# Optimization experiments

Hardware: AMD Instinct MI355X
Metric: run time of the kernel (lower is better)

The kernel has to match this reference:

```python
import jax, jax.numpy as jnp
import numpy as np

N_USER, N_ITEM, D, K, E = 80000, 40000, 128, 10, 2000000

def _mlp(x, w1, b1, w2, b2, w3, b3):
    # MLP from source: linear->tanh->linear->tanh->linear->L2 normalize (eval mode, dropout off)
    x = jnp.tanh(x @ w1 + b1)
    x = jnp.tanh(x @ w2 + b2)
    x = x @ w3 + b3
    return x / jnp.maximum(jnp.linalg.norm(x, axis=-1, keepdims=True), 1e-12)

def setup_inputs() -> dict:
    key = jax.random.key(0)
    ks = jax.random.split(key, 24)
    s = 0.05
    inp = {
        'uemb_s': jax.random.normal(ks[0], (N_USER, D), jnp.float32),
        'iemb_s': jax.random.normal(ks[1], (N_ITEM, D), jnp.float32),
        'uemb_t': jax.random.normal(ks[2], (N_USER, D), jnp.float32),
        'u_emb_sp': jax.random.normal(ks[3], (N_USER, D), jnp.float32),
        'edge_user': jax.random.randint(ks[4], (E,), 0, N_USER, jnp.int32),
        'edge_item': jax.random.randint(ks[5], (E,), 0, N_ITEM, jnp.int32),
        # meta nets
        'Wu': jax.random.normal(ks[6], (4 * D, D), jnp.float32) * s,
        'bu': jnp.zeros((D,), jnp.float32),
        'Wi': jax.random.normal(ks[7], (2 * D, D), jnp.float32) * s,
        'bi': jnp.zeros((D,), jnp.float32),
        # mlp1: D -> D*K -> D//2 -> D*K
        'm1w1': jax.random.normal(ks[8], (D, D * K), jnp.float32) * s,
        'm1b1': jnp.zeros((D * K,), jnp.float32),
        'm1w2': jax.random.normal(ks[9], (D * K, D // 2), jnp.float32) * s,
        'm1b2': jnp.zeros((D // 2,), jnp.float32),
        'm1w3': jax.random.normal(ks[10], (D // 2, D * K), jnp.float32) * s,
        'm1b3': jnp.zeros((D * K,), jnp.float32),
        # mlp2: D -> D*K -> D//2 -> D*K
        'm2w1': jax.random.normal(ks[11], (D, D * K), jnp.float32) * s,
        'm2b1': jnp.zeros((D * K,), jnp.float32),
        'm2w2': jax.random.normal(ks[12], (D * K, D // 2), jnp.float32) * s,
        'm2b2': jnp.zeros((D // 2,), jnp.float32),
        'm2w3': jax.random.normal(ks[13], (D // 2, D * K), jnp.float32) * s,
        'm2b3': jnp.zeros((D * K,), jnp.float32),
    }
    return inp

def reference(uemb_s, iemb_s, uemb_t, u_emb_sp, edge_user, edge_item,
              Wu, bu, Wi, bi,
              m1w1, m1b1, m1w2, m1b2, m1w3, m1b3,
              m2w1, m2b1, m2w2, m2b2, m2w3, m2b3):
    # spmm with all-ones values == gather + segment_sum over the bipartite edge list
    neighbors_u = jax.ops.segment_sum(iemb_s[edge_item], edge_user, num_segments=N_USER)  # [U, D]
    tmp_embu = jax.lax.stop_gradient(
        jnp.concatenate([uemb_s, uemb_t, u_emb_sp, neighbors_u], axis=1)) @ Wu + bu       # [U, D]
    neighbors_i = jax.ops.segment_sum(((uemb_s + u_emb_sp) * 0.5)[edge_user], edge_item,
                                      num_segments=N_ITEM)                               # [I, D]
    tmp_embi = jax.lax.stop_gradient(
        jnp.concatenate([iemb_s, neighbors_i], axis=1)) @ Wi + bi                         # [I, D]
    metau = _mlp(tmp_embu, m1w1, m1b1, m1w2, m1b2, m1w3, m1b3).reshape(-1, D, K)          # [U, D, K]
    metai = _mlp(tmp_embi, m2w1, m2b1, m2w2, m2b2, m2w3, m2b3).reshape(-1, K, D)          # [I, K, D]
    meta_biasu = jnp.mean(metau, axis=0)  # [D, K]
    meta_biasi = jnp.mean(metai, axis=0)  # [K, D]
    low_weightu = jax.nn.softmax(metau + meta_biasu, axis=1)
    low_weighti = jax.nn.softmax(metai + meta_biasi, axis=1)
    return (low_weightu, low_weighti)
```

## Files before the change

kernel.cpp:

```cpp
#include <hip/hip_runtime.h>
#include <hip/hip_bf16.h>

#define D_ 128
#define DK_ 1280
#define K_ 10

typedef __attribute__((ext_vector_type(8))) short bh8;
typedef __attribute__((ext_vector_type(4))) short bh4;
typedef __attribute__((ext_vector_type(4))) float f32x4;

__device__ __forceinline__ short f2b(float f) {
    unsigned u = __builtin_bit_cast(unsigned, f);
    u += 0x7fffu + ((u >> 16) & 1u);
    return (short)(u >> 16);
}
__device__ __forceinline__ float b2f(short s) {
    unsigned u = ((unsigned)(unsigned short)s) << 16;
    return __builtin_bit_cast(float, u);
}
__device__ __forceinline__ float tanh_fast(float x) {
    float e = __expf(2.f * x);
    return 1.f - __fdividef(2.f, e + 1.f);
}
__device__ __forceinline__ f32x4 mfma16(bh8 a, bh8 b, f32x4 c) {
    return __builtin_amdgcn_mfma_f32_16x16x32_bf16(a, b, c, 0, 0, 0);
}

__device__ __forceinline__ int blk_excl_scan(int v, int t) {
    __shared__ int wp[4];
    int lane = t & 63, w = t >> 6;
    int s = v;
    for (int o = 1; o < 64; o <<= 1) {
        int pv = __shfl_up(s, o);
        if (lane >= o) s += pv;
    }
    if (lane == 63) wp[w] = s;
    __syncthreads();
    if (t == 0) {
        int a = 0;
#pragma unroll
        for (int k = 0; k < 4; ++k) { int x = wp[k]; wp[k] = a; a += x; }
    }
    __syncthreads();
    int r = s - v + wp[w];
    __syncthreads();
    return r;
}

__global__ __launch_bounds__(256) void cvt_all(
    const float* __restrict__ us, const float* __restrict__ ut,
    const float* __restrict__ usp, const float* __restrict__ is_,
    short* __restrict__ usb, short* __restrict__ utb,
    short* __restrict__ uspb, short* __restrict__ uavg, short* __restrict__ isb,
    int n4u, int n4i)
{
    int i = blockIdx.x * 256 + threadIdx.x;
    if (i < n4u) {
        float4 a = ((const float4*)us)[i];
        float4 b = ((const float4*)ut)[i];
        float4 c = ((const float4*)usp)[i];
        bh4 sa, sb, sc, sv;
        sa[0] = f2b(a.x); sa[1] = f2b(a.y); sa[2] = f2b(a.z); sa[3] = f2b(a.w);
        sb[0] = f2b(b.x); sb[1] = f2b(b.y); sb[2] = f2b(b.z); sb[3] = f2b(b.w);
        sc[0] = f2b(c.x); sc[1] = f2b(c.y); sc[2] = f2b(c.z); sc[3] = f2b(c.w);
        sv[0] = f2b(0.5f * (a.x + c.x)); sv[1] = f2b(0.5f * (a.y + c.y));
        sv[2] = f2b(0.5f * (a.z + c.z)); sv[3] = f2b(0.5f * (a.w + c.w));
        ((bh4*)usb)[i] = sa; ((bh4*)utb)[i] = sb;
        ((bh4*)uspb)[i] = sc; ((bh4*)uavg)[i] = sv;
    } else if (i < n4u + n4i) {
        int j = i - n4u;
        float4 v = ((const float4*)is_)[j];
        bh4 s;
        s[0] = f2b(v.x); s[1] = f2b(v.y); s[2] = f2b(v.z); s[3] = f2b(v.w);
        ((bh4*)isb)[j] = s;
    }
}

struct PackArgs {
    const float* W[8];
    short* o[8];
    int K[8];
    int N[8];
};
__global__ __launch_bounds__(256) void pack_all(PackArgs pa)
{
    int seg = blockIdx.y;
    int K = pa.K[seg], N = pa.N[seg];
    int total = K * N;
    int o = blockIdx.x * 256 + threadIdx.x;
    if (o >= total) return;
    const float* W = pa.W[seg];
    short* out = pa.o[seg];
    int j    = o & 7;
    int lane = (o >> 3) & 63;
    int rest = o >> 9;
    int KK = K >> 5;
    int kk = rest % KK;
    int tile = rest / KK;
    int k = kk * 32 + (lane >> 4) * 8 + j;
    int n = tile * 16 + (lane & 15);
    out[o] = f2b(W[(size_t)k * N + n]);
}

__global__ __launch_bounds__(256) void bhist_kernel(
    const int* __restrict__ eu, const int* __restrict__ ei,
    int* __restrict__ bcu, int* __restrict__ bci,
    int E, int shu, int shi, int nbu, int nbi)
{
    __shared__ int hu[160], hi[160];
    int t = threadIdx.x;
    int base = blockIdx.x * 4096;
    if (t < 160) { hu[t] = 0; hi[t] = 0; }
    __syncthreads();
    int n = min(4096, E - base);
#pragma unroll 4
    for (int k = 0; k < 16; ++k) {
        int idx = k * 256 + t;
        if (idx < n) {
            atomicAdd(&hu[eu[base + idx] >> shu], 1);
            atomicAdd(&hi[ei[base + idx] >> shi], 1);
        }
    }
    __syncthreads();
    if (t < nbu && hu[t]) atomicAdd(&bcu[t], hu[t]);
    if (t < nbi && hi[t]) atomicAdd(&bci[t], hi[t]);
}

__global__ __launch_bounds__(256) void binit_kernel(
    const int* __restrict__ bcu, int* __restrict__ gcu, int* __restrict__ bbu, int nbu,
    const int* __restrict__ bci, int* __restrict__ gci, int* __restrict__ bbi, int nbi,
    int E)
{
    int t = threadIdx.x;
    {
        int v = (t < nbu) ? bcu[t] : 0;
        int ex = blk_excl_scan(v, t);
        if (t < nbu) { gcu[t] = ex; bbu[t] = ex; }
        if (t == 0) bbu[nbu] = E;
    }
    __syncthreads();
    {
        int v = (t < nbi) ? bci[t] : 0;
        int ex = blk_excl_scan(v, t);
        if (t < nbi) { gci[t] = ex; bbi[t] = ex; }
        if (t == 0) bbi[nbi] = E;
    }
}

__global__ __launch_bounds__(256) void partition_kernel(
    const int* __restrict__ eu, const int* __restrict__ ei,
    int* __restrict__ gcu, int* __restrict__ gci,
    uint2* __restrict__ ebu, uint2* __restrict__ ebi,
    int E, int shu, int shi, int nbu, int nbi)
{
    __shared__ int hu[160], hi[160];
    int t = threadIdx.x;
    int base = blockIdx.x * 4096;
    if (t < 160) { hu[t] = 0; hi[t] = 0; }
    __syncthreads();
    int n = min(4096, E - base);
    int us[16], is_[16];
#pragma unroll 4
    for (int k = 0; k < 16; ++k) {
        int idx = k * 256 + t;
        if (idx < n) {
            us[k] = eu[base + idx];
            is_[k] = ei[base + idx];
            atomicAdd(&hu[us[k] >> shu], 1);
            atomicAdd(&hi[is_[k] >> shi], 1);
        } else us[k] = -1;
    }
    __syncthreads();
    if (t < nbu) { int c = hu[t]; hu[t] = c ? atomicAdd(&gcu[t], c) : 0; }
    if (t < nbi) { int c = hi[t]; hi[t] = c ? atomicAdd(&gci[t], c) : 0; }
    __syncthreads();
#pragma unroll 4
    for (int k = 0; k < 16; ++k) {
        if (us[k] >= 0) {
            int p1 = atomicAdd(&hu[us[k] >> shu], 1);
            ebu[p1] = make_uint2((unsigned)us[k], (unsigned)is_[k]);
            int p2 = atomicAdd(&hi[is_[k] >> shi], 1);
            ebi[p2] = make_uint2((unsigned)is_[k], (unsigned)us[k]);
        }
    }
}

__global__ __launch_bounds__(256) void fill2_all(
    const uint2* __restrict__ ebu, const int* __restrict__ bbu,
    int* __restrict__ off_u, int* __restrict__ end_u, int* __restrict__ adj_u,
    int NBU, int U,
    const uint2* __restrict__ ebi, const int* __restrict__ bbi,
    int* __restrict__ off_i, int* __restrict__ end_i, int* __restrict__ adj_i, int I)
{
    __shared__ int lcnt[512];
    __shared__ int lcur[512];
    bool isU = (int)blockIdx.x < NBU;
    const uint2* ebuf = isU ? ebu : ebi;
    const int* bbase  = isU ? bbu : bbi;
    int* off  = isU ? off_u : off_i;
    int* end_ = isU ? end_u : end_i;
    int* adj  = isU ? adj_u : adj_i;
    int span_sh = isU ? 9 : 8;
    int nrows = isU ? U : I;
    int b = isU ? blockIdx.x : blockIdx.x - NBU;

    int t = threadIdx.x;
    int rbase = b << span_sh;
    int span = min(1 << span_sh, nrows - rbase);
    int regbeg = bbase[b], regend = bbase[b + 1];
    for (int j = t; j < span; j += 256) lcnt[j] = 0;
    __syncthreads();
    for (int e = regbeg + t; e < regend; e += 256)
        atomicAdd(&lcnt[ebuf[e].x - rbase], 1);
    __syncthreads();
    int c0 = (2 * t < span) ? lcnt[2 * t] : 0;
    int c1 = (2 * t + 1 < span) ? lcnt[2 * t + 1] : 0;
    int ex = blk_excl_scan(c0 + c1, t);
    if (2 * t < span) {
        int beg = regbeg + ex;
        off[rbase + 2 * t] = beg;
        end_[rbase + 2 * t] = beg + c0;
        lcur[2 * t] = beg;
    }
    if (2 * t + 1 < span) {
        int beg = regbeg + ex + c0;
        off[rbase + 2 * t + 1] = beg;
        end_[rbase + 2 * t + 1] = beg + c1;
        lcur[2 * t + 1] = beg;
    }
    __syncthreads();
    for (int e = regbeg + t; e < regend; e += 256) {
        uint2 p = ebuf[e];
        int slot = atomicAdd(&lcur[p.x - rbase], 1);
        adj[slot] = (int)p.y;
    }
}

__global__ __launch_bounds__(256) void gather_all(
    const short* __restrict__ embU, const short* __restrict__ embI,
    const int* __restrict__ off_u, const int* __restrict__ end_u, const int* __restrict__ adj_u,
    const int* __restrict__ off_i, const int* __restrict__ end_i, const int* __restrict__ adj_i,
    short* __restrict__ nub, short* __restrict__ nib, int U, int I)
{
    int gw = (blockIdx.x * 256 + threadIdx.x) >> 6;
    int lane = threadIdx.x & 63;
    const short* emb; const int *offp, *endp, *adjp; short* outp; int row;
    if (gw < U)          { emb = embU; offp = off_u; endp = end_u; adjp = adj_u; outp = nub; row = gw; }
    else if (gw < U + I) { emb = embI; offp = off_i; endp = end_i; adjp = adj_i; outp = nib; row = gw - U; }
    else return;

    int beg = offp[row], end = endp[row];
    float ax = 0.f, ay = 0.f;
    int j = beg;
    for (; j + 3 < end; j += 4) {
        unsigned a = *(const unsigned*)(emb + (size_t)adjp[j]     * D_ + lane * 2);
        unsigned b = *(const unsigned*)(emb + (size_t)adjp[j + 1] * D_ + lane * 2);
        unsigned c = *(const unsigned*)(emb + (size_t)adjp[j + 2] * D_ + lane * 2);
        unsigned d = *(const unsigned*)(emb + (size_t)adjp[j + 3] * D_ + lane * 2);
        ax += b2f((short)(a & 0xffff)) + b2f((short)(b & 0xffff))
            + b2f((short)(c & 0xffff)) + b2f((short)(d & 0xffff));
        ay += b2f((short)(a >> 16)) + b2f((short)(b >> 16))
            + b2f((short)(c >> 16)) + b2f((short)(d >> 16));
    }
    for (; j < end; ++j) {
        unsigned a = *(const unsigned*)(emb + (size_t)adjp[j] * D_ + lane * 2);
        ax += b2f((short)(a & 0xffff));
        ay += b2f((short)(a >> 16));
    }
    unsigned o = ((unsigned)(unsigned short)f2b(ay) << 16) | (unsigned short)(unsigned)f2b(ax);
    *(unsigned*)(outp + (size_t)row * D_ + lane * 2) = o;
}

struct MlpArgs {
    const short *uA0, *uA1, *uA2, *uA3;
    const short *iA0, *iA1;
    const short *uWg, *uW1, *uW2, *uW3;
    const short *iWg, *iW1, *iW2, *iW3;
    const float *ubg, *ub1, *ub2, *ub3;
    const float *ibg, *ib1, *ib2, *ib3;
    short *uY, *iY;
    int UB;
};

__global__ __launch_bounds__(256, 4) void fused_mlp_all(MlpArgs P)
{
    __shared__ char pool[27712];
    short* x2   = (short*)pool;
    short* h2   = (short*)(pool + 4352);
    float* wred = (float*)(pool + 6656);
    float* nrms = (float*)(pool + 6912);
    short* xc   = (short*)(pool + 6976);
    short* h1h  = (short*)(pool + 6976);

    const int t = threadIdx.x;
    const int l = t & 63;
    const int w = t >> 6;
    const int lr = l & 15;
    const int lg = l >> 4;

    const bool isU = (int)blockIdx.x < P.UB;
    const int bid = isU ? (int)blockIdx.x : (int)blockIdx.x - P.UB;
    const size_t rb0 = (size_t)bid * 16;
    const int CHSH = isU ? 6 : 5;
    const int KKG  = isU ? 16 : 8;
    const int XST  = isU ? 520 : 264;
    const short* Wg = isU ? P.uWg : P.iWg;
    const short* W1 = isU ? P.uW1 : P.iW1;
    const short* W2 = isU ? P.uW2 : P.iW2;
    const short* W3 = isU ? P.uW3 : P.iW3;
    const float* bg = isU ? P.ubg : P.ibg;
    const float* b1 = isU ? P.ub1 : P.ib1;
    const float* b2 = isU ? P.ub2 : P.ib2;
    const float* b3 = isU ? P.ub3 : P.ib3;
    short* Ybf = isU ? P.uY : P.iY;

    for (int idx = t; idx < (16 << CHSH); idx += 256) {
        int row = idx >> CHSH;
        int slot = idx & ((1 << CHSH) - 1);
        int a = slot >> 4, cs = slot & 15;
        const short* src = isU ? (a == 0 ? P.uA0 : a == 1 ? P.uA1 : a == 2 ? P.uA2 : P.uA3)
                               : (a == 0 ? P.iA0 : P.iA1);
        bh8 v = *(const bh8*)(src + (rb0 + row) * D_ + cs * 8);
        *(bh8*)(xc + row * XST + slot * 8) = v;
    }
    __syncthreads();

    {
        f32x4 a0 = {0,0,0,0}, b0 = a0, a1 = a0, b1v = a0;
        const short* wp = Wg + (size_t)(2 * w) * KKG * 512 + l * 8;
        const short* wq = wp + (size_t)KKG * 512;
        const short* xp = xc + lr * XST + lg * 8;
        for (int kk = 0; kk < KKG; ++kk) {
            bh8 xf = *(const bh8*)xp; xp += 32;
            bh8 w0 = *(const bh8*)wp; wp += 512;
            bh8 w1 = *(const bh8*)wq; wq += 512;
            if (kk & 1) { b0 = mfma16(w0, xf, b0); b1v = mfma16(w1, xf, b1v); }
            else        { a0 = mfma16(w0, xf, a0); a1 = mfma16(w1, xf, a1); }
        }
        float4 c0 = *(const float4*)(bg + (2 * w) * 16 + lg * 4);
        float4 c1 = *(const float4*)(bg + (2 * w + 1) * 16 + lg * 4);
        bh4 p0, p1;
        p0[0] = f2b(a0[0] + b0[0] + c0.x); p0[1] = f2b(a0[1] + b0[1] + c0.y);
        p0[2] = f2b(a0[2] + b0[2] + c0.z); p0[3] = f2b(a0[3] + b0[3] + c0.w);
        p1[0] = f2b(a1[0] + b1v[0] + c1.x); p1[1] = f2b(a1[1] + b1v[1] + c1.y);
        p1[2] = f2b(a1[2] + b1v[2] + c1.z); p1[3] = f2b(a1[3] + b1v[3] + c1.w);
        *(bh4*)(x2 + lr * 136 + (2 * w) * 16 + lg * 4) = p0;
        *(bh4*)(x2 + lr * 136 + (2 * w + 1) * 16 + lg * 4) = p1;
    }
    __syncthreads();

    bh8 xf[4];
#pragma unroll
    for (int kk = 0; kk < 4; ++kk)
        xf[kk] = *(const bh8*)(x2 + lr * 136 + kk * 32 + lg * 8);

    f32x4 c2a = {0,0,0,0}, c2b = c2a;
#pragma unroll 1
    for (int h = 0; h < 2; ++h) {
        const short* wp = W1 + (size_t)(h * 40 + w * 10) * 2048 + l * 8;
        const float* bp = b1 + (h * 40 + w * 10) * 16 + lg * 4;
        short* hp = h1h + lr * 648 + w * 160 + lg * 4;
#pragma unroll 2
        for (int tt = 0; tt < 10; ++tt) {
            f32x4 acc = {0, 0, 0, 0};
#pragma unroll
            for (int kk = 0; kk < 4; ++kk) {
                bh8 wf = *(const bh8*)wp; wp += 512;
                acc = mfma16(wf, xf[kk], acc);
            }
            float4 bv = *(const float4*)bp; bp += 16;
            bh4 pk1;
            pk1[0] = f2b(tanh_fast(acc[0] + bv.x));
            pk1[1] = f2b(tanh_fast(acc[1] + bv.y));
            pk1[2] = f2b(tanh_fast(acc[2] + bv.z));
            pk1[3] = f2b(tanh_fast(acc[3] + bv.w));
            *(bh4*)hp = pk1; hp += 16;
        }
        __syncthreads();
        const short* wp2 = W2 + (size_t)(w * 40 + h * 20) * 512 + l * 8;
        const short* hq = h1h + lr * 648 + lg * 8;
#pragma unroll 4
        for (int kk = 0; kk < 20; ++kk) {
            bh8 hf = *(const bh8*)hq; hq += 32;
            bh8 wf = *(const bh8*)wp2; wp2 += 512;
            if (kk & 1) c2b = mfma16(wf, hf, c2b);
            else        c2a = mfma16(wf, hf, c2a);
        }
        __syncthreads();
    }

    {
        float4 bv = *(const float4*)(b2 + w * 16 + lg * 4);
        bh4 p2;
        p2[0] = f2b(tanh_fast(c2a[0] + c2b[0] + bv.x));
        p2[1] = f2b(tanh_fast(c2a[1] + c2b[1] + bv.y));
        p2[2] = f2b(tanh_fast(c2a[2] + c2b[2] + bv.z));
        p2[3] = f2b(tanh_fast(c2a[3] + c2b[3] + bv.w));
        *(bh4*)(h2 + lr * 72 + w * 16 + lg * 4) = p2;
    }
    __syncthreads();

    bh8 hf0 = *(const bh8*)(h2 + lr * 72 + lg * 8);
    bh8 hf1 = *(const bh8*)(h2 + lr * 72 + 32 + lg * 8);
    bh4 pk[20];
    float ssq = 0.f;
    {
        const short* wp3 = W3 + (size_t)(w * 20) * 1024 + l * 8;
        const float* bp3 = b3 + w * 320 + lg * 4;
#pragma unroll
        for (int tt = 0; tt < 20; ++tt) {
            f32x4 acc = {0, 0, 0, 0};
            bh8 w0 = *(const bh8*)(wp3 + tt * 1024);
            bh8 w1 = *(const bh8*)(wp3 + tt * 1024 + 512);
            acc = mfma16(w0, hf0, acc);
            acc = mfma16(w1, hf1, acc);
            float4 bv = *(const float4*)(bp3 + tt * 16);
            float v0 = acc[0] + bv.x, v1 = acc[1] + bv.y;
            float v2 = acc[2] + bv.z, v3 = acc[3] + bv.w;
            ssq = fmaf(v0, v0, ssq); ssq = fmaf(v1, v1, ssq);
            ssq = fmaf(v2, v2, ssq); ssq = fmaf(v3, v3, ssq);
            bh4 o;
            o[0] = f2b(v0); o[1] = f2b(v1); o[2] = f2b(v2); o[3] = f2b(v3);
            pk[tt] = o;
        }
    }
    ssq += __shfl_xor(ssq, 16);
    ssq += __shfl_xor(ssq, 32);
    if (l < 16) wred[w * 16 + l] = ssq;
    __syncthreads();
    if (t < 16) {
        float s = wred[t] + wred[16 + t] + wred[32 + t] + wred[48 + t];
        nrms[t] = 1.f / fmaxf(sqrtf(s), 1e-12f);
    }
    __syncthreads();

    {
        float nrm = nrms[lr];
        short* dst = Ybf + (rb0 + lr) * DK_ + w * 320 + lg * 4;
#pragma unroll
        for (int tt = 0; tt < 20; ++tt) {
            bh4 pkv = pk[tt];
            bh4 o;
            o[0] = f2b(b2f(pkv[0]) * nrm); o[1] = f2b(b2f(pkv[1]) * nrm);
            o[2] = f2b(b2f(pkv[2]) * nrm); o[3] = f2b(b2f(pkv[3]) * nrm);
            *(bh4*)(dst + tt * 16) = o;
        }
    }
}

__global__ __launch_bounds__(256) void finalize_bias(
    const short* __restrict__ Yu, const short* __restrict__ Yi,
    float* __restrict__ bsu, float* __restrict__ bsi, int U, int I, int NCH)
{
    int z = blockIdx.y;
    const short* Y = z ? Yi : Yu;
    float* dst = z ? bsi : bsu;
    int M = z ? I : U;
    int chunk = (M + NCH - 1) / NCH;
    int r0 = blockIdx.x * chunk;
    int r1 = min(M, r0 + chunk);
    if (r0 >= r1) return;
    int t = threadIdx.x;
    float s0 = 0.f, s1 = 0.f, s2 = 0.f, s3 = 0.f, s4 = 0.f;
    for (int r = r0; r < r1; ++r) {
        const short* row = Y + (size_t)r * DK_;
        s0 += b2f(row[t]);
        s1 += b2f(row[256 + t]);
        s2 += b2f(row[512 + t]);
        s3 += b2f(row[768 + t]);
        s4 += b2f(row[1024 + t]);
    }
    atomicAdd(&dst[t], s0);
    atomicAdd(&dst[256 + t], s1);
    atomicAdd(&dst[512 + t], s2);
    atomicAdd(&dst[768 + t], s3);
    atomicAdd(&dst[1024 + t], s4);
}

__global__ __launch_bounds__(64) void softmax_all(
    const short* __restrict__ Yu, const short* __restrict__ Yi,
    const float* __restrict__ bsu, const float* __restrict__ bsi,
    float invU, float invI,
    float* __restrict__ outu, float* __restrict__ outi, int U, int I)
{
    __shared__ float rowb[DK_];
    int b = blockIdx.x;
    int t = threadIdx.x;
    if (b < U) {
        size_t base = (size_t)b * DK_;
        for (int i = t; i < DK_ / 4; i += 64) {
            uint2 a = ((const uint2*)(Yu + base))[i];
            float4 bv = ((const float4*)bsu)[i];
            rowb[4 * i + 0] = b2f((short)(a.x & 0xffff)) + bv.x * invU;
            rowb[4 * i + 1] = b2f((short)(a.x >> 16))    + bv.y * invU;
            rowb[4 * i + 2] = b2f((short)(a.y & 0xffff)) + bv.z * invU;
            rowb[4 * i + 3] = b2f((short)(a.y >> 16))    + bv.w * invU;
        }
        __syncthreads();
#pragma unroll 1
        for (int k = 0; k < K_; ++k) {
            float v0 = rowb[t * K_ + k];
            float v1 = rowb[(t + 64) * K_ + k];
            float m = fmaxf(v0, v1);
            for (int off = 32; off; off >>= 1) m = fmaxf(m, __shfl_xor(m, off));
            float e0 = expf(v0 - m), e1 = expf(v1 - m);
            float s = e0 + e1;
            for (int off = 32; off; off >>= 1) s += __shfl_xor(s, off);
            float rs = 1.f / s;
            rowb[t * K_ + k] = e0 * rs;
            rowb[(t + 64) * K_ + k] = e1 * rs;
        }
        __syncthreads();
        for (int i = t; i < DK_ / 4; i += 64)
            ((float4*)(outu + base))[i] = ((const float4*)rowb)[i];
    } else {
        int it = b - U;
        if (it >= I) return;
        size_t base = (size_t)it * DK_;
        float v0[K_], v1[K_];
        float m0 = -1e30f, m1 = -1e30f;
#pragma unroll
        for (int k = 0; k < K_; ++k) {
            unsigned a = *(const unsigned*)(Yi + base + k * D_ + 2 * t);
            float2 bv = ((const float2*)(bsi + k * D_))[t];
            v0[k] = b2f((short)(a & 0xffff)) + bv.x * invI;
            v1[k] = b2f((short)(a >> 16))    + bv.y * invI;
            m0 = fmaxf(m0, v0[k]); m1 = fmaxf(m1, v1[k]);
        }
        float s0 = 0.f, s1 = 0.f;
#pragma unroll
        for (int k = 0; k < K_; ++k) {
            v0[k] = expf(v0[k] - m0); s0 += v0[k];
            v1[k] = expf(v1[k] - m1); s1 += v1[k];
        }
        float r0 = 1.f / s0, r1 = 1.f / s1;
#pragma unroll
        for (int k = 0; k < K_; ++k) {
            float2 o; o.x = v0[k] * r0; o.y = v1[k] * r1;
            ((float2*)(outi + base + k * D_))[t] = o;
        }
    }
}

extern "C" void kernel_launch(void* const* d_in, const int* in_sizes, int n_in,
                              void* d_out, int out_size, void* d_ws, size_t ws_size,
                              hipStream_t stream)
{
    const float* uemb_s   = (const float*)d_in[0];
    const float* iemb_s   = (const float*)d_in[1];
    const float* uemb_t   = (const float*)d_in[2];
    const float* u_emb_sp = (const float*)d_in[3];
    const int*   eu       = (const int*)d_in[4];
    const int*   ei       = (const int*)d_in[5];
    const float* Wu  = (const float*)d_in[6];
    const float* bu  = (const float*)d_in[7];
    const float* Wi  = (const float*)d_in[8];
    const float* bi  = (const float*)d_in[9];
    const float* m1w1 = (const float*)d_in[10];
    const float* m1b1 = (const float*)d_in[11];
    const float* m1w2 = (const float*)d_in[12];
    const float* m1b2 = (const float*)d_in[13];
    const float* m1w3 = (const float*)d_in[14];
    const float* m1b3 = (const float*)d_in[15];
    const float* m2w1 = (const float*)d_in[16];
    const float* m2b1 = (const float*)d_in[17];
    const float* m2w2 = (const float*)d_in[18];
    const float* m2b2 = (const float*)d_in[19];
    const float* m2w3 = (const float*)d_in[20];
    const float* m2b3 = (const float*)d_in[21];

    const int U = in_sizes[0] / D_;
    const int I = in_sizes[1] / D_;
    const int E = in_sizes[4];

    const int SHU = 9, SHI = 8;
    const int NBU = (U + 511) >> 9;
    const int NBI = (I + 255) >> 8;
    const int UB = U / 16, IB = I / 16;

    char* p = (char*)d_ws;
    auto alloc = [&](size_t bytes) { char* r = p; p += (bytes + 255) & ~(size_t)255; return r; };

    short* usb  = (short*)alloc((size_t)U * D_ * 2);
    short* utb  = (short*)alloc((size_t)U * D_ * 2);
    short* uspb = (short*)alloc((size_t)U * D_ * 2);
    short* uavg = (short*)alloc((size_t)U * D_ * 2);
    short* isb  = (short*)alloc((size_t)I * D_ * 2);
    short* nub  = (short*)alloc((size_t)U * D_ * 2);
    short* nib  = (short*)alloc((size_t)I * D_ * 2);
    short* ybu  = (short*)alloc((size_t)U * DK_ * 2);
    short* ybi  = (short*)alloc((size_t)I * DK_ * 2);
    short* WgU  = (short*)alloc(512 * 128 * 2);
    short* WgI  = (short*)alloc(256 * 128 * 2);
    short* W1U  = (short*)alloc(128 * 1280 * 2);
    short* W2U  = (short*)alloc(1280 * 64 * 2);
    short* W3U  = (short*)alloc(64 * 1280 * 2);
    short* W1I  = (short*)alloc(128 * 1280 * 2);
    short* W2I  = (short*)alloc(1280 * 64 * 2);
    short* W3I  = (short*)alloc(64 * 1280 * 2);
    int*   zbuf = (int*)alloc((320 + 2 * DK_) * 4);
    int* bcnt_u = zbuf;
    int* bcnt_i = zbuf + 160;
    float* bsu  = (float*)(zbuf + 320);
    float* bsi  = bsu + DK_;
    int* gcur_u = (int*)alloc(160 * 4);
    int* gcur_i = (int*)alloc(160 * 4);
    int* bbase_u = (int*)alloc(161 * 4);
    int* bbase_i = (int*)alloc(161 * 4);
    int* off_u  = (int*)alloc((size_t)U * 4);
    int* end_u  = (int*)alloc((size_t)U * 4);
    int* off_i  = (int*)alloc((size_t)I * 4);
    int* end_i  = (int*)alloc((size_t)I * 4);
    uint2* ebu  = (uint2*)alloc((size_t)E * 8);
    uint2* ebi  = (uint2*)alloc((size_t)E * 8);
    int* adj_u  = (int*)alloc((size_t)E * 4);
    int* adj_i  = (int*)alloc((size_t)E * 4);

    float* outu = (float*)d_out;
    float* outi = outu + (size_t)U * DK_;

    hipMemsetAsync(zbuf, 0, (320 + 2 * DK_) * 4, stream);

    int n4u = U * D_ / 4, n4i = I * D_ / 4;
    cvt_all<<<(n4u + n4i + 255) / 256, 256, 0, stream>>>(
        uemb_s, uemb_t, u_emb_sp, iemb_s, usb, utb, uspb, uavg, isb, n4u, n4i);

    PackArgs pa;
    pa.W[0] = Wu;   pa.o[0] = WgU; pa.K[0] = 512;  pa.N[0] = 128;
    pa.W[1] = Wi;   pa.o[1] = WgI; pa.K[1] = 256;  pa.N[1] = 128;
    pa.W[2] = m1w1; pa.o[2] = W1U; pa.K[2] = 128;  pa.N[2] = 1280;
    pa.W[3] = m1w2; pa.o[3] = W2U; pa.K[3] = 1280; pa.N[3] = 64;
    pa.W[4] = m1w3; pa.o[4] = W3U; pa.K[4] = 64;   pa.N[4] = 1280;
    pa.W[5] = m2w1; pa.o[5] = W1I; pa.K[5] = 128;  pa.N[5] = 1280;
    pa.W[6] = m2w2; pa.o[6] = W2I; pa.K[6] = 1280; pa.N[6] = 64;
    pa.W[7] = m2w3; pa.o[7] = W3I; pa.K[7] = 64;   pa.N[7] = 1280;
    pack_all<<<dim3(640, 8), 256, 0, stream>>>(pa);

    int pb = (E + 4095) / 4096;
    bhist_kernel<<<pb, 256, 0, stream>>>(eu, ei, bcnt_u, bcnt_i, E, SHU, SHI, NBU, NBI);
    binit_kernel<<<1, 256, 0, stream>>>(bcnt_u, gcur_u, bbase_u, NBU,
                                        bcnt_i, gcur_i, bbase_i, NBI, E);
    partition_kernel<<<pb, 256, 0, stream>>>(eu, ei, gcur_u, gcur_i, ebu, ebi,
                                             E, SHU, SHI, NBU, NBI);
    fill2_all<<<NBU + NBI, 256, 0, stream>>>(ebu, bbase_u, off_u, end_u, adj_u, NBU, U,
                                             ebi, bbase_i, off_i, end_i, adj_i, I);

    gather_all<<<(U + I + 3) / 4, 256, 0, stream>>>(
        isb, uavg, off_u, end_u, adj_u, off_i, end_i, adj_i, nub, nib, U, I);

    MlpArgs ma;
    ma.uA0 = usb; ma.uA1 = utb; ma.uA2 = uspb; ma.uA3 = nub;
    ma.iA0 = isb; ma.iA1 = nib;
    ma.uWg = WgU; ma.uW1 = W1U; ma.uW2 = W2U; ma.uW3 = W3U;
    ma.iWg = WgI; ma.iW1 = W1I; ma.iW2 = W2I; ma.iW3 = W3I;
    ma.ubg = bu; ma.ub1 = m1b1; ma.ub2 = m1b2; ma.ub3 = m1b3;
    ma.ibg = bi; ma.ib1 = m2b1; ma.ib2 = m2b2; ma.ib3 = m2b3;
    ma.uY = ybu; ma.iY = ybi;
    ma.UB = UB;
    fused_mlp_all<<<UB + IB, 256, 0, stream>>>(ma);

    finalize_bias<<<dim3(256, 2), 256, 0, stream>>>(ybu, ybi, bsu, bsi, U, I, 256);

    softmax_all<<<U + I, 64, 0, stream>>>(ybu, ybi, bsu, bsi,
                                          1.0f / (float)U, 1.0f / (float)I, outu, outi, U, I);
}
```

Measured before the change: 1.033 ms.

## Process 32 rows per MLP block and defer L2 normalization to consumers

The fused MLP kernel now handles 32 rows per block instead of 16, so each weight fragment loaded from global memory feeds two MFMAs and weight traffic per row is halved. The input staging through shared memory is dropped and A fragments are read straight from global. The per-row inverse norm is written to a separate buffer and applied later in finalize_bias and softmax, which removes the second normalize-and-store pass and the extra barrier. The cost is more LDS per block, which may lower occupancy, half as many blocks, and unnormalized bf16 values in storage.

Result: faster. 929.4 us (-10.0%).

```diff
diff --git a/kernel.cpp b/kernel.cpp
--- a/kernel.cpp
+++ b/kernel.cpp
@@ -279,18 +279,17 @@
     const float *ubg, *ub1, *ub2, *ub3;
     const float *ibg, *ib1, *ib2, *ib3;
     short *uY, *iY;
+    float *uNrm, *iNrm;
     int UB;
 };
 
 __global__ __launch_bounds__(256, 4) void fused_mlp_all(MlpArgs P)
 {
-    __shared__ char pool[27712];
+    __shared__ char pool[35328];
     short* x2   = (short*)pool;
-    short* h2   = (short*)(pool + 4352);
-    float* wred = (float*)(pool + 6656);
-    float* nrms = (float*)(pool + 6912);
-    short* xc   = (short*)(pool + 6976);
-    short* h1h  = (short*)(pool + 6976);
+    short* h1q  = (short*)(pool + 8704);
+    short* h2   = (short*)(pool + 29696);
+    float* wred = (float*)(pool + 34304);
 
     const int t = threadIdx.x;
     const int l = t & 63;
@@ -300,10 +299,8 @@
 
     const bool isU = (int)blockIdx.x < P.UB;
     const int bid = isU ? (int)blockIdx.x : (int)blockIdx.x - P.UB;
-    const size_t rb0 = (size_t)bid * 16;
-    const int CHSH = isU ? 6 : 5;
+    const size_t rb0 = (size_t)bid * 32;
     const int KKG  = isU ? 16 : 8;
-    const int XST  = isU ? 520 : 264;
     const short* Wg = isU ? P.uWg : P.iWg;
     const short* W1 = isU ? P.uW1 : P.iW1;
     const short* W2 = isU ? P.uW2 : P.iW2;
@@ -313,147 +310,156 @@
     const float* b2 = isU ? P.ub2 : P.ib2;
     const float* b3 = isU ? P.ub3 : P.ib3;
     short* Ybf = isU ? P.uY : P.iY;
-
-    for (int idx = t; idx < (16 << CHSH); idx += 256) {
-        int row = idx >> CHSH;
-        int slot = idx & ((1 << CHSH) - 1);
-        int a = slot >> 4, cs = slot & 15;
-        const short* src = isU ? (a == 0 ? P.uA0 : a == 1 ? P.uA1 : a == 2 ? P.uA2 : P.uA3)
-                               : (a == 0 ? P.iA0 : P.iA1);
-        bh8 v = *(const bh8*)(src + (rb0 + row) * D_ + cs * 8);
-        *(bh8*)(xc + row * XST + slot * 8) = v;
-    }
-    __syncthreads();
+    float* Nrm = isU ? P.uNrm : P.iNrm;
+    const short* srcs[4];
+    if (isU) { srcs[0] = P.uA0; srcs[1] = P.uA1; srcs[2] = P.uA2; srcs[3] = P.uA3; }
+    else     { srcs[0] = P.iA0; srcs[1] = P.iA1; srcs[2] = P.iA0; srcs[3] = P.iA1; }
 
     {
-        f32x4 a0 = {0,0,0,0}, b0 = a0, a1 = a0, b1v = a0;
+        f32x4 acc[2][2] = {{{0,0,0,0},{0,0,0,0}},{{0,0,0,0},{0,0,0,0}}};
         const short* wp = Wg + (size_t)(2 * w) * KKG * 512 + l * 8;
         const short* wq = wp + (size_t)KKG * 512;
-        const short* xp = xc + lr * XST + lg * 8;
         for (int kk = 0; kk < KKG; ++kk) {
-            bh8 xf = *(const bh8*)xp; xp += 32;
+            const short* src = srcs[kk >> 2];
+            int coff = (kk & 3) * 32 + lg * 8;
+            bh8 x0 = *(const bh8*)(src + (rb0 + lr) * D_ + coff);
+            bh8 x1 = *(const bh8*)(src + (rb0 + 16 + lr) * D_ + coff);
             bh8 w0 = *(const bh8*)wp; wp += 512;
             bh8 w1 = *(const bh8*)wq; wq += 512;
-            if (kk & 1) { b0 = mfma16(w0, xf, b0); b1v = mfma16(w1, xf, b1v); }
-            else        { a0 = mfma16(w0, xf, a0); a1 = mfma16(w1, xf, a1); }
+            acc[0][0] = mfma16(w0, x0, acc[0][0]);
+            acc[1][0] = mfma16(w0, x1, acc[1][0]);
+            acc[0][1] = mfma16(w1, x0, acc[0][1]);
+            acc[1][1] = mfma16(w1, x1, acc[1][1]);
         }
         float4 c0 = *(const float4*)(bg + (2 * w) * 16 + lg * 4);
         float4 c1 = *(const float4*)(bg + (2 * w + 1) * 16 + lg * 4);
-        bh4 p0, p1;
-        p0[0] = f2b(a0[0] + b0[0] + c0.x); p0[1] = f2b(a0[1] + b0[1] + c0.y);
-        p0[2] = f2b(a0[2] + b0[2] + c0.z); p0[3] = f2b(a0[3] + b0[3] + c0.w);
-        p1[0] = f2b(a1[0] + b1v[0] + c1.x); p1[1] = f2b(a1[1] + b1v[1] + c1.y);
-        p1[2] = f2b(a1[2] + b1v[2] + c1.z); p1[3] = f2b(a1[3] + b1v[3] + c1.w);
-        *(bh4*)(x2 + lr * 136 + (2 * w) * 16 + lg * 4) = p0;
-        *(bh4*)(x2 + lr * 136 + (2 * w + 1) * 16 + lg * 4) = p1;
-    }
-    __syncthreads();
-
-    bh8 xf[4];
-#pragma unroll
-    for (int kk = 0; kk < 4; ++kk)
-        xf[kk] = *(const bh8*)(x2 + lr * 136 + kk * 32 + lg * 8);
-
-    f32x4 c2a = {0,0,0,0}, c2b = c2a;
+#pragma unroll
+        for (int rg = 0; rg < 2; ++rg) {
+            bh4 p0, p1;
+            p0[0] = f2b(acc[rg][0][0] + c0.x); p0[1] = f2b(acc[rg][0][1] + c0.y);
+            p0[2] = f2b(acc[rg][0][2] + c0.z); p0[3] = f2b(acc[rg][0][3] + c0.w);
+            p1[0] = f2b(acc[rg][1][0] + c1.x); p1[1] = f2b(acc[rg][1][1] + c1.y);
+            p1[2] = f2b(acc[rg][1][2] + c1.z); p1[3] = f2b(acc[rg][1][3] + c1.w);
+            *(bh4*)(x2 + (rg * 16 + lr) * 136 + (2 * w) * 16 + lg * 4) = p0;
+            *(bh4*)(x2 + (rg * 16 + lr) * 136 + (2 * w + 1) * 16 + lg * 4) = p1;
+        }
+    }
+    __syncthreads();
+
+    bh8 xf[2][4];
+#pragma unroll
+    for (int rg = 0; rg < 2; ++rg)
+#pragma unroll
+        for (int kk = 0; kk < 4; ++kk)
+            xf[rg][kk] = *(const bh8*)(x2 + (rg * 16 + lr) * 136 + kk * 32 + lg * 8);
+
+    f32x4 c2[2][2] = {{{0,0,0,0},{0,0,0,0}},{{0,0,0,0},{0,0,0,0}}};
 #pragma unroll 1
-    for (int h = 0; h < 2; ++h) {
-        const short* wp = W1 + (size_t)(h * 40 + w * 10) * 2048 + l * 8;
-        const float* bp = b1 + (h * 40 + w * 10) * 16 + lg * 4;
-        short* hp = h1h + lr * 648 + w * 160 + lg * 4;
-#pragma unroll 2
-        for (int tt = 0; tt < 10; ++tt) {
-            f32x4 acc = {0, 0, 0, 0};
+    for (int q = 0; q < 4; ++q) {
+        const short* wp = W1 + (size_t)(q * 20 + w * 5) * 2048 + l * 8;
+        const float* bp = b1 + (q * 20 + w * 5) * 16 + lg * 4;
+#pragma unroll 1
+        for (int tt = 0; tt < 5; ++tt) {
+            f32x4 a0 = {0,0,0,0}, a1 = a0;
 #pragma unroll
             for (int kk = 0; kk < 4; ++kk) {
                 bh8 wf = *(const bh8*)wp; wp += 512;
-                acc = mfma16(wf, xf[kk], acc);
+                a0 = mfma16(wf, xf[0][kk], a0);
+                a1 = mfma16(wf, xf[1][kk], a1);
             }
             float4 bv = *(const float4*)bp; bp += 16;
-            bh4 pk1;
-            pk1[0] = f2b(tanh_fast(acc[0] + bv.x));
-            pk1[1] = f2b(tanh_fast(acc[1] + bv.y));
-            pk1[2] = f2b(tanh_fast(acc[2] + bv.z));
-            pk1[3] = f2b(tanh_fast(acc[3] + bv.w));
-            *(bh4*)hp = pk1; hp += 16;
+            bh4 pk0, pk1;
+            pk0[0] = f2b(tanh_fast(a0[0] + bv.x)); pk0[1] = f2b(tanh_fast(a0[1] + bv.y));
+            pk0[2] = f2b(tanh_fast(a0[2] + bv.z)); pk0[3] = f2b(tanh_fast(a0[3] + bv.w));
+            pk1[0] = f2b(tanh_fast(a1[0] + bv.x)); pk1[1] = f2b(tanh_fast(a1[1] + bv.y));
+            pk1[2] = f2b(tanh_fast(a1[2] + bv.z)); pk1[3] = f2b(tanh_fast(a1[3] + bv.w));
+            int lt = w * 5 + tt;
+            *(bh4*)(h1q + lr * 328 + lt * 16 + lg * 4) = pk0;
+            *(bh4*)(h1q + (16 + lr) * 328 + lt * 16 + lg * 4) = pk1;
         }
         __syncthreads();
-        const short* wp2 = W2 + (size_t)(w * 40 + h * 20) * 512 + l * 8;
-        const short* hq = h1h + lr * 648 + lg * 8;
-#pragma unroll 4
-        for (int kk = 0; kk < 20; ++kk) {
-            bh8 hf = *(const bh8*)hq; hq += 32;
+        const short* wp2 = W2 + (size_t)(w * 40 + q * 10) * 512 + l * 8;
+        const short* hq0 = h1q + lr * 328 + lg * 8;
+        const short* hq1 = h1q + (16 + lr) * 328 + lg * 8;
+#pragma unroll 2
+        for (int kk = 0; kk < 10; ++kk) {
             bh8 wf = *(const bh8*)wp2; wp2 += 512;
-            if (kk & 1) c2b = mfma16(wf, hf, c2b);
-            else        c2a = mfma16(wf, hf, c2a);
+            bh8 h0 = *(const bh8*)(hq0 + kk * 32);
+            bh8 h1v = *(const bh8*)(hq1 + kk * 32);
+            if (kk & 1) { c2[0][1] = mfma16(wf, h0, c2[0][1]); c2[1][1] = mfma16(wf, h1v, c2[1][1]); }
+            else        { c2[0][0] = mfma16(wf, h0, c2[0][0]); c2[1][0] = mfma16(wf, h1v, c2[1][0]); }
         }
         __syncthreads();
     }
 
     {
         float4 bv = *(const float4*)(b2 + w * 16 + lg * 4);
-        bh4 p2;
-        p2[0] = f2b(tanh_fast(c2a[0] + c2b[0] + bv.x));
-        p2[1] = f2b(tanh_fast(c2a[1] + c2b[1] + bv.y));
-        p2[2] = f2b(tanh_fast(c2a[2] + c2b[2] + bv.z));
-        p2[3] = f2b(tanh_fast(c2a[3] + c2b[3] + bv.w));
-        *(bh4*)(h2 + lr * 72 + w * 16 + lg * 4) = p2;
-    }
-    __syncthreads();
-
-    bh8 hf0 = *(const bh8*)(h2 + lr * 72 + lg * 8);
-    bh8 hf1 = *(const bh8*)(h2 + lr * 72 + 32 + lg * 8);
-    bh4 pk[20];
-    float ssq = 0.f;
+#pragma unroll
+        for (int rg = 0; rg < 2; ++rg) {
+            bh4 p2;
+            p2[0] = f2b(tanh_fast(c2[rg][0][0] + c2[rg][1][0] + bv.x));
+            p2[1] = f2b(tanh_fast(c2[rg][0][1] + c2[rg][1][1] + bv.y));
+            p2[2] = f2b(tanh_fast(c2[rg][0][2] + c2[rg][1][2] + bv.z));
+            p2[3] = f2b(tanh_fast(c2[rg][0][3] + c2[rg][1][3] + bv.w));
+            *(bh4*)(h2 + (rg * 16 + lr) * 72 + w * 16 + lg * 4) = p2;
+        }
+    }
+    __syncthreads();
+
     {
+        bh8 hf[2][2];
+#pragma unroll
+        for (int rg = 0; rg < 2; ++rg) {
+            hf[rg][0] = *(const bh8*)(h2 + (rg * 16 + lr) * 72 + lg * 8);
+            hf[rg][1] = *(const bh8*)(h2 + (rg * 16 + lr) * 72 + 32 + lg * 8);
+        }
+        float ssq0 = 0.f, ssq1 = 0.f;
         const short* wp3 = W3 + (size_t)(w * 20) * 1024 + l * 8;
         const float* bp3 = b3 + w * 320 + lg * 4;
-#pragma unroll
+        short* dst0 = Ybf + (rb0 + lr) * DK_ + w * 320 + lg * 4;
+        short* dst1 = Ybf + (rb0 + 16 + lr) * DK_ + w * 320 + lg * 4;
+#pragma unroll 2
         for (int tt = 0; tt < 20; ++tt) {
-            f32x4 acc = {0, 0, 0, 0};
             bh8 w0 = *(const bh8*)(wp3 + tt * 1024);
             bh8 w1 = *(const bh8*)(wp3 + tt * 1024 + 512);
-            acc = mfma16(w0, hf0, acc);
-            acc = mfma16(w1, hf1, acc);
             float4 bv = *(const float4*)(bp3 + tt * 16);
-            float v0 = acc[0] + bv.x, v1 = acc[1] + bv.y;
-            float v2 = acc[2] + bv.z, v3 = acc[3] + bv.w;
-            ssq = fmaf(v0, v0, ssq); ssq = fmaf(v1, v1, ssq);
-            ssq = fmaf(v2, v2, ssq); ssq = fmaf(v3, v3, ssq);
-            bh4 o;
-            o[0] = f2b(v0); o[1] = f2b(v1); o[2] = f2b(v2); o[3] = f2b(v3);
-            pk[tt] = o;
-        }
-    }
-    ssq += __shfl_xor(ssq, 16);
-    ssq += __shfl_xor(ssq, 32);
-    if (l < 16) wred[w * 16 + l] = ssq;
-    __syncthreads();
-    if (t < 16) {
-        float s = wred[t] + wred[16 + t] + wred[32 + t] + wred[48 + t];
-        nrms[t] = 1.f / fmaxf(sqrtf(s), 1e-12f);
-    }
-    __syncthreads();
-
-    {
-        float nrm = nrms[lr];
-        short* dst = Ybf + (rb0 + lr) * DK_ + w * 320 + lg * 4;
-#pragma unroll
-        for (int tt = 0; tt < 20; ++tt) {
-            bh4 pkv = pk[tt];
-            bh4 o;
-            o[0] = f2b(b2f(pkv[0]) * nrm); o[1] = f2b(b2f(pkv[1]) * nrm);
-            o[2] = f2b(b2f(pkv[2]) * nrm); o[3] = f2b(b2f(pkv[3]) * nrm);
-            *(bh4*)(dst + tt * 16) = o;
-        }
+            f32x4 a0 = {0,0,0,0}, a1 = a0;
+            a0 = mfma16(w0, hf[0][0], a0); a0 = mfma16(w1, hf[0][1], a0);
+            a1 = mfma16(w0, hf[1][0], a1); a1 = mfma16(w1, hf[1][1], a1);
+            float v00 = a0[0] + bv.x, v01 = a0[1] + bv.y, v02 = a0[2] + bv.z, v03 = a0[3] + bv.w;
+            float v10 = a1[0] + bv.x, v11 = a1[1] + bv.y, v12 = a1[2] + bv.z, v13 = a1[3] + bv.w;
+            ssq0 = fmaf(v00, v00, ssq0); ssq0 = fmaf(v01, v01, ssq0);
+            ssq0 = fmaf(v02, v02, ssq0); ssq0 = fmaf(v03, v03, ssq0);
+            ssq1 = fmaf(v10, v10, ssq1); ssq1 = fmaf(v11, v11, ssq1);
+            ssq1 = fmaf(v12, v12, ssq1); ssq1 = fmaf(v13, v13, ssq1);
+            bh4 o0, o1;
+            o0[0] = f2b(v00); o0[1] = f2b(v01); o0[2] = f2b(v02); o0[3] = f2b(v03);
+            o1[0] = f2b(v10); o1[1] = f2b(v11); o1[2] = f2b(v12); o1[3] = f2b(v13);
+            *(bh4*)(dst0 + tt * 16) = o0;
+            *(bh4*)(dst1 + tt * 16) = o1;
+        }
+        ssq0 += __shfl_xor(ssq0, 16); ssq0 += __shfl_xor(ssq0, 32);
+        ssq1 += __shfl_xor(ssq1, 16); ssq1 += __shfl_xor(ssq1, 32);
+        if (l < 16) {
+            wred[w * 32 + l] = ssq0;
+            wred[w * 32 + 16 + l] = ssq1;
+        }
+    }
+    __syncthreads();
+    if (t < 32) {
+        float s = wred[t] + wred[32 + t] + wred[64 + t] + wred[96 + t];
+        Nrm[rb0 + t] = 1.f / fmaxf(sqrtf(s), 1e-12f);
     }
 }
 
 __global__ __launch_bounds__(256) void finalize_bias(
     const short* __restrict__ Yu, const short* __restrict__ Yi,
+    const float* __restrict__ nrmU, const float* __restrict__ nrmI,
     float* __restrict__ bsu, float* __restrict__ bsi, int U, int I, int NCH)
 {
     int z = blockIdx.y;
     const short* Y = z ? Yi : Yu;
+    const float* nr = z ? nrmI : nrmU;
     float* dst = z ? bsi : bsu;
     int M = z ? I : U;
     int chunk = (M + NCH - 1) / NCH;
@@ -464,11 +470,12 @@
     float s0 = 0.f, s1 = 0.f, s2 = 0.f, s3 = 0.f, s4 = 0.f;
     for (int r = r0; r < r1; ++r) {
         const short* row = Y + (size_t)r * DK_;
-        s0 += b2f(row[t]);
-        s1 += b2f(row[256 + t]);
-        s2 += b2f(row[512 + t]);
-        s3 += b2f(row[768 + t]);
-        s4 += b2f(row[1024 + t]);
+        float nv = nr[r];
+        s0 += b2f(row[t]) * nv;
+        s1 += b2f(row[256 + t]) * nv;
+        s2 += b2f(row[512 + t]) * nv;
+        s3 += b2f(row[768 + t]) * nv;
+        s4 += b2f(row[1024 + t]) * nv;
     }
     atomicAdd(&dst[t], s0);
     atomicAdd(&dst[256 + t], s1);
@@ -479,6 +486,7 @@
 
 __global__ __launch_bounds__(64) void softmax_all(
     const short* __restrict__ Yu, const short* __restrict__ Yi,
+    const float* __restrict__ nrmU, const float* __restrict__ nrmI,
     const float* __restrict__ bsu, const float* __restrict__ bsi,
     float invU, float invI,
     float* __restrict__ outu, float* __restrict__ outi, int U, int I)
@@ -488,13 +496,14 @@
     int t = threadIdx.x;
     if (b < U) {
         size_t base = (size_t)b * DK_;
+        float nrm = nrmU[b];
         for (int i = t; i < DK_ / 4; i += 64) {
             uint2 a = ((const uint2*)(Yu + base))[i];
             float4 bv = ((const float4*)bsu)[i];
-            rowb[4 * i + 0] = b2f((short)(a.x & 0xffff)) + bv.x * invU;
-            rowb[4 * i + 1] = b2f((short)(a.x >> 16))    + bv.y * invU;
-            rowb[4 * i + 2] = b2f((short)(a.y & 0xffff)) + bv.z * invU;
-            rowb[4 * i + 3] = b2f((short)(a.y >> 16))    + bv.w * invU;
+            rowb[4 * i + 0] = b2f((short)(a.x & 0xffff)) * nrm + bv.x * invU;
+            rowb[4 * i + 1] = b2f((short)(a.x >> 16))    * nrm + bv.y * invU;
+            rowb[4 * i + 2] = b2f((short)(a.y & 0xffff)) * nrm + bv.z * invU;
+            rowb[4 * i + 3] = b2f((short)(a.y >> 16))    * nrm + bv.w * invU;
         }
         __syncthreads();
 #pragma unroll 1
@@ -517,14 +526,15 @@
         int it = b - U;
         if (it >= I) return;
         size_t base = (size_t)it * DK_;
+        float nrm = nrmI[it];
         float v0[K_], v1[K_];
         float m0 = -1e30f, m1 = -1e30f;
 #pragma unroll
         for (int k = 0; k < K_; ++k) {
             unsigned a = *(const unsigned*)(Yi + base + k * D_ + 2 * t);
             float2 bv = ((const float2*)(bsi + k * D_))[t];
-            v0[k] = b2f((short)(a & 0xffff)) + bv.x * invI;
-            v1[k] = b2f((short)(a >> 16))    + bv.y * invI;
+            v0[k] = b2f((short)(a & 0xffff)) * nrm + bv.x * invI;
+            v1[k] = b2f((short)(a >> 16))    * nrm + bv.y * invI;
             m0 = fmaxf(m0, v0[k]); m1 = fmaxf(m1, v1[k]);
         }
         float s0 = 0.f, s1 = 0.f;
@@ -576,7 +586,7 @@
     const int SHU = 9, SHI = 8;
     const int NBU = (U + 511) >> 9;
     const int NBI = (I + 255) >> 8;
-    const int UB = U / 16, IB = I / 16;
+    const int UB = U / 32, IB = I / 32;
 
     char* p = (char*)d_ws;
     auto alloc = [&](size_t bytes) { char* r = p; p += (bytes + 255) & ~(size_t)255; return r; };
@@ -590,6 +600,8 @@
     short* nib  = (short*)alloc((size_t)I * D_ * 2);
     short* ybu  = (short*)alloc((size_t)U * DK_ * 2);
     short* ybi  = (short*)alloc((size_t)I * DK_ * 2);
+    float* nrmU = (float*)alloc((size_t)U * 4);
+    float* nrmI = (float*)alloc((size_t)I * 4);
     short* WgU  = (short*)alloc(512 * 128 * 2);
     short* WgI  = (short*)alloc(256 * 128 * 2);
     short* W1U  = (short*)alloc(128 * 1280 * 2);
@@ -656,11 +668,12 @@
     ma.ubg = bu; ma.ub1 = m1b1; ma.ub2 = m1b2; ma.ub3 = m1b3;
     ma.ibg = bi; ma.ib1 = m2b1; ma.ib2 = m2b2; ma.ib3 = m2b3;
     ma.uY = ybu; ma.iY = ybi;
+    ma.uNrm = nrmU; ma.iNrm = nrmI;
     ma.UB = UB;
     fused_mlp_all<<<UB + IB, 256, 0, stream>>>(ma);
 
-    finalize_bias<<<dim3(256, 2), 256, 0, stream>>>(ybu, ybi, bsu, bsi, U, I, 256);
-
-    softmax_all<<<U + I, 64, 0, stream>>>(ybu, ybi, bsu, bsi,
+    finalize_bias<<<dim3(256, 2), 256, 0, stream>>>(ybu, ybi, nrmU, nrmI, bsu, bsi, U, I, 256);
+
+    softmax_all<<<U + I, 64, 0, stream>>>(ybu, ybi, nrmU, nrmI, bsu, bsi,
                                           1.0f / (float)U, 1.0f / (float)I, outu, outi, U, I);
 }
```
